# Performance work log

Hardware: AMD Instinct MI355X
Metric: run time of the kernel (lower is better)

Reference implementation:

```python
import jax, jax.numpy as jnp
import numpy as np

N = 100000      # num_nodes
R = 8           # num_relations
D = 128         # node feature size
EMB = 128       # embedding_size
E = 1600000     # num edges
B = 16384       # batch of triples


def setup_inputs() -> dict:
    key = jax.random.key(0)
    ks = jax.random.split(key, 10)
    edge_src = jax.random.randint(ks[0], (E,), 0, N, dtype=jnp.int32)
    edge_dst = jax.random.randint(ks[1], (E,), 0, N, dtype=jnp.int32)
    edge_rel = jax.random.randint(ks[2], (E,), 0, R, dtype=jnp.int32)
    tri_nodes = jax.random.randint(ks[3], (B, 2), 0, N, dtype=jnp.int32)
    tri_rel = jax.random.randint(ks[4], (B,), 0, R, dtype=jnp.int32)
    X = jax.random.normal(ks[5], (N, D), dtype=jnp.float32)            # frozen node features
    W_rel = jax.random.normal(ks[6], (R, D, EMB), dtype=jnp.float32) * (1.0 / np.sqrt(D))
    W_self = jax.random.normal(ks[7], (D, EMB), dtype=jnp.float32) * (1.0 / np.sqrt(D))
    b = jnp.zeros((EMB,), dtype=jnp.float32)
    rel_emb = jax.random.normal(ks[8], (R, EMB), dtype=jnp.float32) * (1.0 / np.sqrt(EMB))  # xavier-ish
    return {"X": X, "W_rel": W_rel, "W_self": W_self, "b": b, "rel_emb": rel_emb,
            "edge_src": edge_src, "edge_dst": edge_dst, "edge_rel": edge_rel,
            "tri_nodes": tri_nodes, "tri_rel": tri_rel}


def _rgcn_layer(X, W_rel, W_self, b, edge_src, edge_dst, edge_rel):
    # per-relation transformed features: [R, N, EMB]
    XW = jnp.einsum('nd,rde->rne', X, W_rel)
    # gather per-edge messages: [E, EMB]
    msg = XW[edge_rel, edge_src]
    # RGCN normalization 1/c_{i,r}: count of (dst, rel) pairs
    comb = edge_dst.astype(jnp.int32) * R + edge_rel
    cnt = jax.ops.segment_sum(jnp.ones_like(comb, dtype=jnp.float32), comb, num_segments=N * R)
    norm = 1.0 / jnp.maximum(cnt[comb], 1.0)
    agg = jax.ops.segment_sum(msg * norm[:, None], edge_dst, num_segments=N)  # [N, EMB]
    return jax.nn.relu(agg + X @ W_self + b)


def reference(X, W_rel, W_self, b, rel_emb, edge_src, edge_dst, edge_rel, tri_nodes, tri_rel):
    H = _rgcn_layer(X, W_rel, W_self, b, edge_src, edge_dst, edge_rel)  # [N, EMB]
    subj = H[tri_nodes[:, 0]]          # [B, EMB]
    obj = H[tri_nodes[:, 1]]           # [B, EMB]
    rel = rel_emb[tri_rel]             # [B, EMB]
    scores = jnp.sum(subj * rel * obj, axis=1, keepdims=True)  # [B, 1]
    return scores
```

## Files before the change

kernel.cpp:

```cpp
#include <hip/hip_runtime.h>

typedef float f32x4 __attribute__((ext_vector_type(4)));
typedef short bf16x8 __attribute__((ext_vector_type(8)));

__device__ __forceinline__ unsigned short f2bf(float f) {
  unsigned int u = __float_as_uint(f);
  u += 0x7FFFu + ((u >> 16) & 1u);
  return (unsigned short)(u >> 16);
}
__device__ __forceinline__ float bflo(unsigned int u) {
  return __uint_as_float(u << 16);
}
__device__ __forceinline__ float bfhi(unsigned int u) {
  return __uint_as_float(u & 0xFFFF0000u);
}

__global__ __launch_bounds__(256) void k_init(int4* __restrict__ map4, int n4,
                                              int* __restrict__ counter,
                                              int4* __restrict__ cnt4, int m4) {
  int i = blockIdx.x * 256 + threadIdx.x;
  int4 neg1 = make_int4(-1, -1, -1, -1);
  int4 zero = make_int4(0, 0, 0, 0);
  if (i < m4) cnt4[i] = zero;
  if (i < n4) map4[i] = neg1;
  if (i < 64) counter[i] = 0;
}

__global__ void k_build_map(const int* __restrict__ tri_nodes, int* __restrict__ map,
                            int* __restrict__ uniq, int* __restrict__ counter, int n) {
  int i = blockIdx.x * blockDim.x + threadIdx.x;
  if (i >= n) return;
  int node = tri_nodes[i];
  int old = atomicCAS(&map[node], -1, -2);
  if (old == -1) {
    int mid = atomicAdd(counter, 1);
    uniq[mid] = node;
    map[node] = mid;
  }
}

__global__ void k_count(const int* __restrict__ esrc, const int* __restrict__ edst,
                        const int* __restrict__ erel, const int* __restrict__ map,
                        int* __restrict__ cnt_c, int E,
                        const float* __restrict__ X, unsigned short* __restrict__ X16,
                        int total8, int2* __restrict__ c_pk, int* __restrict__ wcount) {
  int t = threadIdx.x;
  int i = blockIdx.x * 256 + t;
  if (i < total8) {
    const float4* s = (const float4*)(X + (size_t)i * 8);
    float4 v0 = s[0], v1 = s[1];
    uint4 p;
    p.x = (unsigned int)f2bf(v0.x) | ((unsigned int)f2bf(v0.y) << 16);
    p.y = (unsigned int)f2bf(v0.z) | ((unsigned int)f2bf(v0.w) << 16);
    p.z = (unsigned int)f2bf(v1.x) | ((unsigned int)f2bf(v1.y) << 16);
    p.w = (unsigned int)f2bf(v1.z) | ((unsigned int)f2bf(v1.w) << 16);
    ((uint4*)X16)[i] = p;
  }
  bool valid = false;
  int comb = 0, src = 0;
  if (i < E) {
    int mid = map[edst[i]];
    if (mid >= 0) {
      valid = true;
      comb = mid * 8 + erel[i];
      src = esrc[i];
      atomicAdd(&cnt_c[comb], 1);
    }
  }
  unsigned long long m = __ballot(valid);
  int lane = t & 63;
  int w = (blockIdx.x << 2) + (t >> 6);
  if (valid) {
    int rank = (int)__popcll(m & ((1ull << lane) - 1ull));
    c_pk[w * 64 + rank] = make_int2(comb, src);
  }
  if (lane == 0) wcount[w] = (int)__popcll(m);
}

__global__ __launch_bounds__(256) void k_scan_s1(const int* __restrict__ cnt_c,
                                                 int* __restrict__ bsum) {
  __shared__ int sh[256];
  int tid = threadIdx.x;
  int base = blockIdx.x * 1024 + tid * 4;
  int s = cnt_c[base] + cnt_c[base + 1] + cnt_c[base + 2] + cnt_c[base + 3];
  sh[tid] = s;
  __syncthreads();
  for (int o = 1; o < 256; o <<= 1) {
    int x = (tid >= o) ? sh[tid - o] : 0;
    __syncthreads();
    sh[tid] += x;
    __syncthreads();
  }
  if (tid == 255) bsum[blockIdx.x] = sh[255];
}

__global__ __launch_bounds__(256) void k_scan_s3(const int* __restrict__ cnt_c,
                                                 const int* __restrict__ bsum,
                                                 int* __restrict__ seg_start,
                                                 int* __restrict__ seg_ofs, int M) {
  __shared__ int sh[256];
  int tid = threadIdx.x;
  int bv = bsum[tid];
  sh[tid] = bv;
  __syncthreads();
  for (int o = 1; o < 256; o <<= 1) {
    int x = (tid >= o) ? sh[tid - o] : 0;
    __syncthreads();
    sh[tid] += x;
    __syncthreads();
  }
  int incl_at_blk = sh[blockIdx.x];
  int total = sh[255];
  __syncthreads();
  int blk_off = incl_at_blk - bsum[blockIdx.x];
  if (blockIdx.x == 0 && tid == 0) seg_start[M] = total;
  int base = blockIdx.x * 1024 + tid * 4;
  int c0 = cnt_c[base], c1 = cnt_c[base + 1], c2 = cnt_c[base + 2], c3 = cnt_c[base + 3];
  int s = c0 + c1 + c2 + c3;
  sh[tid] = s;
  __syncthreads();
  for (int o = 1; o < 256; o <<= 1) {
    int x = (tid >= o) ? sh[tid - o] : 0;
    __syncthreads();
    sh[tid] += x;
    __syncthreads();
  }
  int run = blk_off + sh[tid] - s;
  seg_start[base] = run; seg_ofs[base] = run; run += c0;
  seg_start[base + 1] = run; seg_ofs[base + 1] = run; run += c1;
  seg_start[base + 2] = run; seg_ofs[base + 2] = run; run += c2;
  seg_start[base + 3] = run; seg_ofs[base + 3] = run;
}

__global__ void k_scw(const float* __restrict__ W_rel, const float* __restrict__ W_self,
                      unsigned short* __restrict__ Wf,
                      const int2* __restrict__ c_pk, const int* __restrict__ wcount,
                      int* __restrict__ seg_ofs, int* __restrict__ s_src, int nwaves) {
  int t = threadIdx.x;
  int i = blockIdx.x * 256 + t;
  if (i < 9 * 16384) {
    int j = i & 7;
    int tmp = i >> 3;
    int col = tmp & 127;
    int ku = (tmp >> 7) & 15;
    int r = tmp >> 11;
    int d = ku * 8 + j;
    float v = (r < 8) ? W_rel[r * 16384 + d * 128 + col] : W_self[d * 128 + col];
    Wf[i] = f2bf(v);
  }
  int w = blockIdx.x * 4 + (t >> 6);
  if (w < nwaves) {
    int lane = t & 63;
    if (lane < wcount[w]) {
      int2 p = c_pk[w * 64 + lane];
      int pos = atomicAdd(&seg_ofs[p.x], 1);
      s_src[pos] = p.y;
    }
  }
}

__global__ void k_cvt_w(const float* __restrict__ W_rel, const float* __restrict__ W_self,
                        unsigned short* __restrict__ Wf) {
  int i = blockIdx.x * 256 + threadIdx.x;
  if (i >= 9 * 16384) return;
  int j = i & 7;
  int tmp = i >> 3;
  int col = tmp & 127;
  int ku = (tmp >> 7) & 15;
  int r = tmp >> 11;
  int d = ku * 8 + j;
  float v = (r < 8) ? W_rel[r * 16384 + d * 128 + col] : W_self[d * 128 + col];
  Wf[i] = f2bf(v);
}
__global__ void k_scatter(const int* __restrict__ esrc, const int* __restrict__ edst,
                          const int* __restrict__ erel, const int* __restrict__ map,
                          int* __restrict__ seg_ofs, int* __restrict__ s_src, int E) {
  int i = blockIdx.x * blockDim.x + threadIdx.x;
  if (i >= E) return;
  int mid = map[edst[i]];
  if (mid >= 0) {
    int comb = mid * 8 + erel[i];
    int pos = atomicAdd(&seg_ofs[comb], 1);
    s_src[pos] = esrc[i];
  }
}

template <int XMODE>
__global__ __launch_bounds__(256) void k_fused(
    const float* __restrict__ X, const unsigned short* __restrict__ X16,
    const unsigned short* __restrict__ Wf, const float* __restrict__ bvec,
    const int* __restrict__ uniq, const int* __restrict__ counter,
    const int* __restrict__ seg_start, const int* __restrict__ s_src,
    float* __restrict__ Hacc) {
  __shared__ __align__(16) unsigned short a_lds[16 * 128];
  __shared__ int lds_src[768];

  int nm = *counter;
  int mid0 = blockIdx.x * 16;
  if (mid0 >= nm) return;

  int t = threadIdx.x;
  int er = t >> 4, seg = t & 15;
  int lane = t & 63, l15 = lane & 15, lg = lane >> 4;
  int wc = t >> 6;
  int mid = mid0 + er;

  int i0 = seg_start[mid0 * 8];
  int range = seg_start[mid0 * 8 + 128] - i0;
  for (int j = t; j < range && j < 768; j += 256) lds_src[j] = s_src[i0 + j];
  bool fits = (range <= 768);

  f32x4 acc[2];
  {
    f32x4 z = {0.f, 0.f, 0.f, 0.f};
    acc[0] = z; acc[1] = z;
  }

  for (int r = 0; r < 9; ++r) {
    __syncthreads();

    {
      float aa[8];
#pragma unroll
      for (int q = 0; q < 8; ++q) aa[q] = 0.f;

      auto addrow = [&](int sidx) {
        if (XMODE == 0) {
          const float4* xr = (const float4*)(X + (size_t)sidx * 128) + seg * 2;
          float4 v0 = xr[0], v1 = xr[1];
          aa[0] += v0.x; aa[1] += v0.y; aa[2] += v0.z; aa[3] += v0.w;
          aa[4] += v1.x; aa[5] += v1.y; aa[6] += v1.z; aa[7] += v1.w;
        } else {
          uint4 u = *(const uint4*)(X16 + (size_t)sidx * 128 + seg * 8);
          aa[0] += bflo(u.x); aa[1] += bfhi(u.x);
          aa[2] += bflo(u.y); aa[3] += bfhi(u.y);
          aa[4] += bflo(u.z); aa[5] += bfhi(u.z);
          aa[6] += bflo(u.w); aa[7] += bfhi(u.w);
        }
      };

      if (r < 8) {
        int comb = mid * 8 + r;
        int s0 = seg_start[comb], s1 = seg_start[comb + 1];
        int cnt = s1 - s0;
        if (fits) {
          int o = s0 - i0, oe = s1 - i0;
          for (; o + 2 <= oe; o += 2) {
            int ia = lds_src[o], ib = lds_src[o + 1];
            addrow(ia);
            addrow(ib);
          }
          if (o < oe) addrow(lds_src[o]);
        } else {
          int e = s0;
          for (; e + 2 <= s1; e += 2) {
            int ia = s_src[e], ib = s_src[e + 1];
            addrow(ia);
            addrow(ib);
          }
          if (e < s1) addrow(s_src[e]);
        }
        if (cnt > 1) {
          float sc = 1.0f / (float)cnt;
#pragma unroll
          for (int q = 0; q < 8; ++q) aa[q] *= sc;
        }
      } else if (mid < nm) {
        addrow(uniq[mid]);
      }
      uint4 p;
      p.x = (unsigned int)f2bf(aa[0]) | ((unsigned int)f2bf(aa[1]) << 16);
      p.y = (unsigned int)f2bf(aa[2]) | ((unsigned int)f2bf(aa[3]) << 16);
      p.z = (unsigned int)f2bf(aa[4]) | ((unsigned int)f2bf(aa[5]) << 16);
      p.w = (unsigned int)f2bf(aa[6]) | ((unsigned int)f2bf(aa[7]) << 16);
      *(uint4*)&a_lds[(((er * 16 + seg) ^ (er & 7)) * 8)] = p;
    }
    __syncthreads();

    const unsigned short* wf = Wf + r * 16384;
#pragma unroll
    for (int kb = 0; kb < 4; ++kb) {
      int ku = kb * 4 + lg;
      bf16x8 af = *(const bf16x8*)&a_lds[((l15 * 16 + ku) ^ (l15 & 7)) * 8];
#pragma unroll
      for (int n = 0; n < 2; ++n) {
        int col = wc * 32 + n * 16 + l15;
        bf16x8 bfr = *(const bf16x8*)(wf + ((size_t)(ku * 128 + col)) * 8);
        acc[n] = __builtin_amdgcn_mfma_f32_16x16x32_bf16(af, bfr, acc[n], 0, 0, 0);
      }
    }
  }

#pragma unroll
  for (int n = 0; n < 2; ++n) {
    int col = wc * 32 + n * 16 + l15;
    float bv = bvec[col];
#pragma unroll
    for (int q = 0; q < 4; ++q) {
      int row = mid0 + lg * 4 + q;
      float v = acc[n][q] + bv;
      Hacc[(size_t)row * 128 + col] = v > 0.f ? v : 0.f;
    }
  }
}

__global__ void k_score(const float* __restrict__ H, const int* __restrict__ map,
                        const float* __restrict__ rel_emb, const int* __restrict__ tri_nodes,
                        const int* __restrict__ tri_rel, float* __restrict__ out, int B) {
  int w = (blockIdx.x * blockDim.x + threadIdx.x) >> 6;
  int lane = threadIdx.x & 63;
  if (w >= B) return;
  int s = map[tri_nodes[w * 2]];
  int o = map[tri_nodes[w * 2 + 1]];
  const float* hs = H + (size_t)s * 128;
  const float* ho = H + (size_t)o * 128;
  const float* rr = rel_emb + (size_t)tri_rel[w] * 128;
  float p = hs[lane] * ho[lane] * rr[lane] + hs[lane + 64] * ho[lane + 64] * rr[lane + 64];
#pragma unroll
  for (int ofs = 32; ofs > 0; ofs >>= 1) p += __shfl_down(p, ofs);
  if (lane == 0) out[w] = p;
}

extern "C" void kernel_launch(void* const* d_in, const int* in_sizes, int n_in,
                              void* d_out, int out_size, void* d_ws, size_t ws_size,
                              hipStream_t stream) {
  const float* X       = (const float*)d_in[0];
  const float* W_rel   = (const float*)d_in[1];
  const float* W_self  = (const float*)d_in[2];
  const float* bvec    = (const float*)d_in[3];
  const float* rel_emb = (const float*)d_in[4];
  const int* edge_src  = (const int*)d_in[5];
  const int* edge_dst  = (const int*)d_in[6];
  const int* edge_rel  = (const int*)d_in[7];
  const int* tri_nodes = (const int*)d_in[8];
  const int* tri_rel   = (const int*)d_in[9];

  int N  = in_sizes[0] / 128;
  int E  = in_sizes[5];
  int nt = in_sizes[8];
  int B  = in_sizes[9];
  int M  = nt * 8;
  int eblocks = (E + 255) / 256;
  int nwaves = eblocks * 4;

  char* ws = (char*)d_ws;
  int* map       = (int*)ws;
  int* counter   = map + N;
  int* uniq      = counter + 64;
  int* cnt_c     = uniq + nt;
  int* seg_start = cnt_c + M;
  int* seg_ofs   = seg_start + M + 64;
  int* bsum      = seg_ofs + M;
  int* wcount    = bsum + 256;
  int* s_src     = wcount + nwaves + 64;
  float* Hacc    = (float*)(s_src + E);
  unsigned short* Wf  = (unsigned short*)cnt_c;
  unsigned short* X16 = (unsigned short*)(Hacc + (size_t)nt * 128);
  int2* c_pk = (int2*)(X16 + (size_t)N * 128);
  size_t need_big = ((char*)(c_pk + E)) - ws;
  bool bigws = ws_size >= need_big;

  k_init<<<256, 256, 0, stream>>>((int4*)map, N / 4, counter, (int4*)cnt_c, M / 4);
  k_build_map<<<(nt + 255) / 256, 256, 0, stream>>>(tri_nodes, map, uniq, counter, nt);
  if (bigws) {
    k_count<<<eblocks, 256, 0, stream>>>(edge_src, edge_dst, edge_rel, map, cnt_c, E,
                                         X, X16, N * 16, c_pk, wcount);
  } else {
    k_count<<<eblocks, 256, 0, stream>>>(edge_src, edge_dst, edge_rel, map, cnt_c, E,
                                         X, (unsigned short*)Hacc , 0,
                                         (int2*)Hacc ,
                                         wcount);
  }
  k_scan_s1<<<256, 256, 0, stream>>>(cnt_c, bsum);
  k_scan_s3<<<256, 256, 0, stream>>>(cnt_c, bsum, seg_start, seg_ofs, M);
  if (bigws) {
    k_scw<<<eblocks, 256, 0, stream>>>(W_rel, W_self, Wf, c_pk, wcount, seg_ofs,
                                       s_src, nwaves);
    k_fused<1><<<nt / 16, 256, 0, stream>>>(X, X16, Wf, bvec, uniq, counter,
                                            seg_start, s_src, Hacc);
  } else {
    k_cvt_w<<<(9 * 16384 + 255) / 256, 256, 0, stream>>>(W_rel, W_self, Wf);
    k_scatter<<<eblocks, 256, 0, stream>>>(edge_src, edge_dst, edge_rel, map, seg_ofs,
                                           s_src, E);
    k_fused<0><<<nt / 16, 256, 0, stream>>>(X, X16, Wf, bvec, uniq, counter,
                                            seg_start, s_src, Hacc);
  }
  k_score<<<(B * 64 + 255) / 256, 256, 0, stream>>>(Hacc, map, rel_emb, tri_nodes,
                                                    tri_rel, (float*)d_out, B);
}
```

Baseline: 119.9 us.

## Split neighbor gather across two thread halves in fused RGCN kernel

Doubles the fused kernel's block to 512 threads and splits each (node, relation) segment's neighbor-row gather between two halves, each taking every other edge. The second half writes its partial sums to a new shared buffer and the first half combines them, normalizes, and writes the bf16 tile for MFMA. Only the first 256 threads run the MFMA and the output store. The aim is more memory-level parallelism in the latency-bound gather. In exchange it adds an extra barrier and shared-memory traffic per relation step, and half the threads sit idle during the MFMA phase.

Measured after the change: 134.8 us. +12.4%, slower.

```diff
diff --git a/kernel.cpp b/kernel.cpp
--- a/kernel.cpp
+++ b/kernel.cpp
@@ -186,7 +186,7 @@
 }
 
 template <int XMODE>
-__global__ __launch_bounds__(256) void k_fused(
+__global__ __launch_bounds__(512) void k_fused(
     const float* __restrict__ X, const unsigned short* __restrict__ X16,
     const unsigned short* __restrict__ Wf, const float* __restrict__ bvec,
     const int* __restrict__ uniq, const int* __restrict__ counter,
@@ -194,20 +194,23 @@
     float* __restrict__ Hacc) {
   __shared__ __align__(16) unsigned short a_lds[16 * 128];
   __shared__ int lds_src[768];
+  __shared__ float comb_lds[256 * 9];
 
   int nm = *counter;
   int mid0 = blockIdx.x * 16;
   if (mid0 >= nm) return;
 
   int t = threadIdx.x;
-  int er = t >> 4, seg = t & 15;
+  int half = t >> 8;
+  int tl = t & 255;
+  int er = tl >> 4, seg = tl & 15;
   int lane = t & 63, l15 = lane & 15, lg = lane >> 4;
   int wc = t >> 6;
   int mid = mid0 + er;
 
   int i0 = seg_start[mid0 * 8];
   int range = seg_start[mid0 * 8 + 128] - i0;
-  for (int j = t; j < range && j < 768; j += 256) lds_src[j] = s_src[i0 + j];
+  for (int j = t; j < range && j < 768; j += 512) lds_src[j] = s_src[i0 + j];
   bool fits = (range <= 768);
 
   f32x4 acc[2];
@@ -219,54 +222,64 @@
   for (int r = 0; r < 9; ++r) {
     __syncthreads();
 
-    {
-      float aa[8];
-#pragma unroll
-      for (int q = 0; q < 8; ++q) aa[q] = 0.f;
-
-      auto addrow = [&](int sidx) {
-        if (XMODE == 0) {
-          const float4* xr = (const float4*)(X + (size_t)sidx * 128) + seg * 2;
-          float4 v0 = xr[0], v1 = xr[1];
-          aa[0] += v0.x; aa[1] += v0.y; aa[2] += v0.z; aa[3] += v0.w;
-          aa[4] += v1.x; aa[5] += v1.y; aa[6] += v1.z; aa[7] += v1.w;
-        } else {
-          uint4 u = *(const uint4*)(X16 + (size_t)sidx * 128 + seg * 8);
-          aa[0] += bflo(u.x); aa[1] += bfhi(u.x);
-          aa[2] += bflo(u.y); aa[3] += bfhi(u.y);
-          aa[4] += bflo(u.z); aa[5] += bfhi(u.z);
-          aa[6] += bflo(u.w); aa[7] += bfhi(u.w);
+    float aa[8];
+#pragma unroll
+    for (int q = 0; q < 8; ++q) aa[q] = 0.f;
+
+    auto addrow = [&](int sidx) {
+      if (XMODE == 0) {
+        const float4* xr = (const float4*)(X + (size_t)sidx * 128) + seg * 2;
+        float4 v0 = xr[0], v1 = xr[1];
+        aa[0] += v0.x; aa[1] += v0.y; aa[2] += v0.z; aa[3] += v0.w;
+        aa[4] += v1.x; aa[5] += v1.y; aa[6] += v1.z; aa[7] += v1.w;
+      } else {
+        uint4 u = *(const uint4*)(X16 + (size_t)sidx * 128 + seg * 8);
+        aa[0] += bflo(u.x); aa[1] += bfhi(u.x);
+        aa[2] += bflo(u.y); aa[3] += bfhi(u.y);
+        aa[4] += bflo(u.z); aa[5] += bfhi(u.z);
+        aa[6] += bflo(u.w); aa[7] += bfhi(u.w);
+      }
+    };
+
+    int cnt = 0;
+    if (r < 8) {
+      int comb = mid * 8 + r;
+      int s0 = seg_start[comb], s1 = seg_start[comb + 1];
+      cnt = s1 - s0;
+      if (fits) {
+        int o = (s0 - i0) + half, oe = s1 - i0;
+        for (; o + 2 < oe; o += 4) {
+          int ia = lds_src[o], ib = lds_src[o + 2];
+          addrow(ia);
+          addrow(ib);
         }
-      };
-
-      if (r < 8) {
-        int comb = mid * 8 + r;
-        int s0 = seg_start[comb], s1 = seg_start[comb + 1];
-        int cnt = s1 - s0;
-        if (fits) {
-          int o = s0 - i0, oe = s1 - i0;
-          for (; o + 2 <= oe; o += 2) {
-            int ia = lds_src[o], ib = lds_src[o + 1];
-            addrow(ia);
-            addrow(ib);
-          }
-          if (o < oe) addrow(lds_src[o]);
-        } else {
-          int e = s0;
-          for (; e + 2 <= s1; e += 2) {
-            int ia = s_src[e], ib = s_src[e + 1];
-            addrow(ia);
-            addrow(ib);
-          }
-          if (e < s1) addrow(s_src[e]);
+        if (o < oe) addrow(lds_src[o]);
+      } else {
+        int e = s0 + half;
+        for (; e + 2 < s1; e += 4) {
+          int ia = s_src[e], ib = s_src[e + 2];
+          addrow(ia);
+          addrow(ib);
         }
-        if (cnt > 1) {
-          float sc = 1.0f / (float)cnt;
-#pragma unroll
-          for (int q = 0; q < 8; ++q) aa[q] *= sc;
-        }
-      } else if (mid < nm) {
-        addrow(uniq[mid]);
+        if (e < s1) addrow(s_src[e]);
+      }
+    } else if (half == 0 && mid < nm) {
+      addrow(uniq[mid]);
+    }
+
+    if (half == 1) {
+#pragma unroll
+      for (int q = 0; q < 8; ++q) comb_lds[tl * 9 + q] = aa[q];
+    }
+    __syncthreads();
+
+    if (half == 0) {
+#pragma unroll
+      for (int q = 0; q < 8; ++q) aa[q] += comb_lds[tl * 9 + q];
+      if (cnt > 1) {
+        float sc = 1.0f / (float)cnt;
+#pragma unroll
+        for (int q = 0; q < 8; ++q) aa[q] *= sc;
       }
       uint4 p;
       p.x = (unsigned int)f2bf(aa[0]) | ((unsigned int)f2bf(aa[1]) << 16);
@@ -277,29 +290,33 @@
     }
     __syncthreads();
 
-    const unsigned short* wf = Wf + r * 16384;
-#pragma unroll
-    for (int kb = 0; kb < 4; ++kb) {
-      int ku = kb * 4 + lg;
-      bf16x8 af = *(const bf16x8*)&a_lds[((l15 * 16 + ku) ^ (l15 & 7)) * 8];
-#pragma unroll
-      for (int n = 0; n < 2; ++n) {
-        int col = wc * 32 + n * 16 + l15;
-        bf16x8 bfr = *(const bf16x8*)(wf + ((size_t)(ku * 128 + col)) * 8);
-        acc[n] = __builtin_amdgcn_mfma_f32_16x16x32_bf16(af, bfr, acc[n], 0, 0, 0);
+    if (t < 256) {
+      const unsigned short* wf = Wf + r * 16384;
+#pragma unroll
+      for (int kb = 0; kb < 4; ++kb) {
+        int ku = kb * 4 + lg;
+        bf16x8 af = *(const bf16x8*)&a_lds[((l15 * 16 + ku) ^ (l15 & 7)) * 8];
+#pragma unroll
+        for (int n = 0; n < 2; ++n) {
+          int col = wc * 32 + n * 16 + l15;
+          bf16x8 bfr = *(const bf16x8*)(wf + ((size_t)(ku * 128 + col)) * 8);
+          acc[n] = __builtin_amdgcn_mfma_f32_16x16x32_bf16(af, bfr, acc[n], 0, 0, 0);
+        }
       }
     }
   }
 
-#pragma unroll
-  for (int n = 0; n < 2; ++n) {
-    int col = wc * 32 + n * 16 + l15;
-    float bv = bvec[col];
-#pragma unroll
-    for (int q = 0; q < 4; ++q) {
-      int row = mid0 + lg * 4 + q;
-      float v = acc[n][q] + bv;
-      Hacc[(size_t)row * 128 + col] = v > 0.f ? v : 0.f;
+  if (t < 256) {
+#pragma unroll
+    for (int n = 0; n < 2; ++n) {
+      int col = wc * 32 + n * 16 + l15;
+      float bv = bvec[col];
+#pragma unroll
+      for (int q = 0; q < 4; ++q) {
+        int row = mid0 + lg * 4 + q;
+        float v = acc[n][q] + bv;
+        Hacc[(size_t)row * 128 + col] = v > 0.f ? v : 0.f;
+      }
     }
   }
 }
@@ -376,13 +393,13 @@
   if (bigws) {
     k_scw<<<eblocks, 256, 0, stream>>>(W_rel, W_self, Wf, c_pk, wcount, seg_ofs,
                                        s_src, nwaves);
-    k_fused<1><<<nt / 16, 256, 0, stream>>>(X, X16, Wf, bvec, uniq, counter,
+    k_fused<1><<<nt / 16, 512, 0, stream>>>(X, X16, Wf, bvec, uniq, counter,
                                             seg_start, s_src, Hacc);
   } else {
     k_cvt_w<<<(9 * 16384 + 255) / 256, 256, 0, stream>>>(W_rel, W_self, Wf);
     k_scatter<<<eblocks, 256, 0, stream>>>(edge_src, edge_dst, edge_rel, map, seg_ofs,
                                            s_src, E);
-    k_fused<0><<<nt / 16, 256, 0, stream>>>(X, X16, Wf, bvec, uniq, counter,
+    k_fused<0><<<nt / 16, 512, 0, stream>>>(X, X16, Wf, bvec, uniq, counter,
                                             seg_start, s_src, Hacc);
   }
   k_score<<<(B * 64 + 255) / 256, 256, 0, stream>>>(Hacc, map, rel_emb, tri_nodes,
```
